# Kernel optimization log

Measured on AMD Instinct MI355X. Metric: run time of the kernel, lower is better.

The kernel has to match this reference:

```python
import jax, jax.numpy as jnp
import numpy as np

N_NODES = 50000
N_EDGES = 800000
IN_DIM, H1, H2 = 512, 128, 64


def setup_inputs() -> dict:
    key = jax.random.key(0)
    k1, k2, k3, k4 = jax.random.split(key, 4)
    x = jax.random.normal(k1, (N_NODES, IN_DIM), dtype=jnp.float32)
    edge_index = jax.random.randint(k2, (2, N_EDGES), 0, N_NODES, dtype=jnp.int64)
    # Glorot-ish scaled weights (PyG GCNConv uses glorot init)
    W1 = jax.random.normal(k3, (IN_DIM, H1), dtype=jnp.float32) * (1.0 / np.sqrt(IN_DIM))
    b1 = jnp.zeros((H1,), dtype=jnp.float32)
    W2 = jax.random.normal(k4, (H1, H2), dtype=jnp.float32) * (1.0 / np.sqrt(H1))
    b2 = jnp.zeros((H2,), dtype=jnp.float32)
    return {"x": x, "edge_index": edge_index, "W1": W1, "b1": b1, "W2": W2, "b2": b2}


def reference(x, edge_index, W1, b1, W2, b2):
    N = x.shape[0]
    # PyG GCNConv default: add self-loops + symmetric normalization
    loop = jnp.arange(N, dtype=edge_index.dtype)
    src = jnp.concatenate([edge_index[0], loop])  # message source j
    dst = jnp.concatenate([edge_index[1], loop])  # aggregation target i
    deg = jax.ops.segment_sum(jnp.ones(src.shape[0], dtype=x.dtype), dst, num_segments=N)
    dinv = jnp.where(deg > 0, jax.lax.rsqrt(deg), 0.0)
    norm = dinv[src] * dinv[dst]  # [E+N]

    def gcn_relu(h, W, b):
        h = h @ W                                   # [N, F_out]
        msg = h[src] * norm[:, None]                # gather + edge scaling
        agg = jax.ops.segment_sum(msg, dst, num_segments=N)  # scatter-add
        return jax.nn.relu(agg + b)

    h = gcn_relu(x, W1, b1)
    return gcn_relu(h, W2, b2)
```

## Files before the change

kernel.cpp:

```cpp
#include <hip/hip_runtime.h>


constexpr int IN_DIM = 512;
constexpr int HD1 = 128;
constexpr int HD2 = 64;

typedef __attribute__((ext_vector_type(8))) short bf16x8;
typedef __attribute__((ext_vector_type(8))) unsigned short u16x8;
typedef __attribute__((ext_vector_type(4))) float f32x4;
typedef unsigned int u32;

__device__ inline unsigned short f2bf(float f) {
    u32 u = __builtin_bit_cast(u32, f);
    return (unsigned short)((u + 0x7fffu + ((u >> 16) & 1u)) >> 16);
}
__device__ inline float bf_lo(u32 v) { return __builtin_bit_cast(float, v << 16); }
__device__ inline float bf_hi(u32 v) { return __builtin_bit_cast(float, v & 0xffff0000u); }

__device__ inline int elem_off(int row, int k) {
    return (row << 6) + (k ^ ((row & 7) << 3));
}
__device__ inline int elem_off128(int row, int k) {
    return (row << 7) + (k ^ ((row & 7) << 3));
}

__global__ __launch_bounds__(256) void k_zero(int* __restrict__ deg, int N) {
    int i = blockIdx.x * 256 + threadIdx.x;
    if (i < N) deg[i] = 0;
}

__global__ __launch_bounds__(256) void k_prep(const int* __restrict__ dst, int E,
                                              int* __restrict__ deg,
                                              int* __restrict__ rank,
                                              const float* __restrict__ W1,
                                              unsigned short* __restrict__ Wt,
                                              const float* __restrict__ W2,
                                              unsigned short* __restrict__ Wt2) {
    int id = blockIdx.x * 256 + threadIdx.x;
    if (id < E) rank[id] = atomicAdd(&deg[dst[id]], 1);
    if (id < IN_DIM * HD1) {
        int n = id >> 9, k = id & 511;
        Wt[id] = f2bf(W1[k * HD1 + n]);
    }
    if (id < HD1 * HD2) {
        int n = id >> 7, k = id & 127;
        Wt2[id] = f2bf(W2[k * HD2 + n]);
    }
}

__global__ __launch_bounds__(256) void k_dinv_bsum(const int* __restrict__ deg, int N,
                                                   float* __restrict__ dinv,
                                                   int* __restrict__ bsum) {
    __shared__ int s[256];
    int t = threadIdx.x;
    int i = blockIdx.x * 256 + t;
    int d = (i < N) ? deg[i] : 0;
    if (i < N) dinv[i] = rsqrtf((float)(d + 1));
    s[t] = d;
    __syncthreads();
    for (int st = 128; st > 0; st >>= 1) {
        if (t < st) s[t] += s[t + st];
        __syncthreads();
    }
    if (t == 0) bsum[blockIdx.x] = s[0];
}

__global__ __launch_bounds__(256) void k_scan_final(const int* __restrict__ deg, int N,
                                                    const int* __restrict__ bsum, int nb,
                                                    int* __restrict__ rowptr) {
    __shared__ int sb[256];
    __shared__ int s[256];
    int t = threadIdx.x;
    sb[t] = (t < nb) ? bsum[t] : 0;
    __syncthreads();
    for (int off = 1; off < 256; off <<= 1) {
        int v = (t >= off) ? sb[t - off] : 0;
        __syncthreads();
        sb[t] += v;
        __syncthreads();
    }
    int base = (blockIdx.x == 0) ? 0 : sb[blockIdx.x - 1];

    int i = blockIdx.x * 256 + t;
    int v = (i < N) ? deg[i] : 0;
    s[t] = v;
    __syncthreads();
    for (int off = 1; off < 256; off <<= 1) {
        int u = (t >= off) ? s[t - off] : 0;
        __syncthreads();
        s[t] += u;
        __syncthreads();
    }
    int incl = s[t] + base;
    if (i < N) rowptr[i] = incl - v;
    if (i == N - 1) rowptr[N] = incl;
}

__global__ __launch_bounds__(256) void k_mega(const float* __restrict__ X,
                                              const unsigned short* __restrict__ Wt,
                                              unsigned short* __restrict__ H, int N,
                                              int gemmBlocks,
                                              const int* __restrict__ src,
                                              const int* __restrict__ dst, int E,
                                              const int* __restrict__ rowptr,
                                              const int* __restrict__ rank,
                                              int* __restrict__ col) {
    __shared__ unsigned short As[32 * 64];
    __shared__ unsigned short Bs[128 * 64];

    if (blockIdx.x >= gemmBlocks) {
        const int T = (gridDim.x - gemmBlocks) * 256;
        for (int e = (blockIdx.x - gemmBlocks) * 256 + threadIdx.x; e < E; e += T) {
            int d = dst[e];
            col[rowptr[d] + rank[e]] = src[e];
        }
        return;
    }

    const int tid = threadIdx.x;
    const int lane = tid & 63;
    const int wid = tid >> 6;
    const int brow = blockIdx.x * 32;
    const int wr0 = (wid >> 1) * 16;
    const int wc0 = (wid & 1) * 64;
    const bool full = (brow + 32 <= N);

    f32x4 acc[4];
#pragma unroll
    for (int j = 0; j < 4; j++) acc[j] = (f32x4){0.f, 0.f, 0.f, 0.f};

    for (int kt = 0; kt < IN_DIM / 64; kt++) {
        const int k0 = kt * 64;
#pragma unroll
        for (int p = 0; p < 4; p++) {
            int chunk = (wid * 4 + p) * 64 + lane;
            int n = chunk >> 3;
            int kcs = chunk & 7;
            int kc = kcs ^ (n & 7);
            const unsigned short* srcp = &Wt[(size_t)n * IN_DIM + k0 + kc * 8];
            unsigned short* dstp = &Bs[(wid * 4 + p) * 512];
            __builtin_amdgcn_global_load_lds(
                (const __attribute__((address_space(1))) u32*)(const void*)srcp,
                (__attribute__((address_space(3))) u32*)(void*)dstp, 16, 0, 0);
        }
        {
            int r = tid >> 3;
            int kc = tid & 7;
            const float* xp = &X[(size_t)(brow + r) * IN_DIM + k0 + kc * 8];
            float4 v0, v1;
            if (full || (brow + r) < N) {
                v0 = *(const float4*)xp;
                v1 = *(const float4*)(xp + 4);
            } else {
                v0 = make_float4(0.f, 0.f, 0.f, 0.f); v1 = v0;
            }
            u16x8 w;
            w[0] = f2bf(v0.x); w[1] = f2bf(v0.y); w[2] = f2bf(v0.z); w[3] = f2bf(v0.w);
            w[4] = f2bf(v1.x); w[5] = f2bf(v1.y); w[6] = f2bf(v1.z); w[7] = f2bf(v1.w);
            *(u16x8*)&As[elem_off(r, kc * 8)] = w;
        }
        __syncthreads();

#pragma unroll
        for (int kk = 0; kk < 2; kk++) {
            const int kel = kk * 32 + (lane >> 4) * 8;
            bf16x8 a = *(const bf16x8*)&As[elem_off(wr0 + (lane & 15), kel)];
            bf16x8 b[4];
#pragma unroll
            for (int ni = 0; ni < 4; ni++)
                b[ni] = *(const bf16x8*)&Bs[elem_off(wc0 + ni * 16 + (lane & 15), kel)];
#pragma unroll
            for (int ni = 0; ni < 4; ni++)
                acc[ni] = __builtin_amdgcn_mfma_f32_16x16x32_bf16(a, b[ni], acc[ni], 0, 0, 0);
        }
        __syncthreads();
    }

#pragma unroll
    for (int reg = 0; reg < 4; reg++) {
        int grow = brow + wr0 + (lane >> 4) * 4 + reg;
        if (grow < N) {
#pragma unroll
            for (int ni = 0; ni < 4; ni++) {
                int gcol = wc0 + ni * 16 + (lane & 15);
                H[(size_t)grow * HD1 + gcol] = f2bf(acc[ni][reg]);
            }
        }
    }
}

__global__ __launch_bounds__(256) void k_gather1(const unsigned short* __restrict__ h,
                                                 const int* __restrict__ rowptr,
                                                 const int* __restrict__ col,
                                                 const float* __restrict__ dinv,
                                                 const float* __restrict__ bias,
                                                 unsigned short* __restrict__ out, int N) {
    const int i = (blockIdx.x * 256 + threadIdx.x) >> 6;
    const int lane = threadIdx.x & 63;
    if (i >= N) return;
    const int half = lane >> 5;
    const int c4 = (lane & 31) * 4;
    const float di = dinv[i];
    const unsigned short* hc = h + c4;

    float a0 = 0.f, a1 = 0.f, a2 = 0.f, a3 = 0.f;
    if (half == 0) {
        uint2 sv = *(const uint2*)&hc[(size_t)i * HD1];
        float s = di * di;
        a0 = bf_lo(sv.x) * s; a1 = bf_hi(sv.x) * s;
        a2 = bf_lo(sv.y) * s; a3 = bf_hi(sv.y) * s;
    }
    const int beg = rowptr[i], end = rowptr[i + 1];
    for (int p0 = beg; p0 < end; p0 += 64) {
        int idx = p0 + lane;
        bool okl = idx < end;
        int myj = okl ? col[idx] : i;
        float mydj = okl ? dinv[myj] : 0.f;
        const int cnt8 = (min(64, end - p0) + 7) & ~7;
        uint2 v[4]; float wv[4];
#pragma unroll
        for (int q = 0; q < 4; q++) {
            int e = 2 * q + half;
            int j = __shfl(myj, e);
            wv[q] = __shfl(mydj, e) * di;
            v[q] = *(const uint2*)&hc[(size_t)j * HD1];
        }
        for (int k = 8; k < cnt8; k += 8) {
            uint2 nv[4]; float nw[4];
#pragma unroll
            for (int q = 0; q < 4; q++) {
                int e = k + 2 * q + half;
                int j = __shfl(myj, e);
                nw[q] = __shfl(mydj, e) * di;
                nv[q] = *(const uint2*)&hc[(size_t)j * HD1];
            }
#pragma unroll
            for (int q = 0; q < 4; q++) {
                a0 = fmaf(bf_lo(v[q].x), wv[q], a0);
                a1 = fmaf(bf_hi(v[q].x), wv[q], a1);
                a2 = fmaf(bf_lo(v[q].y), wv[q], a2);
                a3 = fmaf(bf_hi(v[q].y), wv[q], a3);
            }
#pragma unroll
            for (int q = 0; q < 4; q++) { v[q] = nv[q]; wv[q] = nw[q]; }
        }
#pragma unroll
        for (int q = 0; q < 4; q++) {
            a0 = fmaf(bf_lo(v[q].x), wv[q], a0);
            a1 = fmaf(bf_hi(v[q].x), wv[q], a1);
            a2 = fmaf(bf_lo(v[q].y), wv[q], a2);
            a3 = fmaf(bf_hi(v[q].y), wv[q], a3);
        }
    }
    a0 += __shfl_xor(a0, 32);
    a1 += __shfl_xor(a1, 32);
    a2 += __shfl_xor(a2, 32);
    a3 += __shfl_xor(a3, 32);
    if (half == 0) {
        float4 bv = *(const float4*)&bias[c4];
        u32 w0 = (u32)f2bf(fmaxf(a0 + bv.x, 0.f)) | ((u32)f2bf(fmaxf(a1 + bv.y, 0.f)) << 16);
        u32 w1 = (u32)f2bf(fmaxf(a2 + bv.z, 0.f)) | ((u32)f2bf(fmaxf(a3 + bv.w, 0.f)) << 16);
        *(uint2*)&out[(size_t)i * HD1 + c4] = make_uint2(w0, w1);
    }
}

__global__ __launch_bounds__(256) void k_gemm2(const unsigned short* __restrict__ A,
                                               const unsigned short* __restrict__ Wt2,
                                               unsigned short* __restrict__ H, int N) {
    __shared__ unsigned short As[128 * 128];
    __shared__ unsigned short Bs[64 * 128];
    const int tid = threadIdx.x;
    const int lane = tid & 63;
    const int wid = tid >> 6;
    const int brow = blockIdx.x * 128;
    const int wr0 = wid * 32;

#pragma unroll
    for (int p = 0; p < 8; p++) {
        int chunk = (wid * 8 + p) * 64 + lane;
        int r = chunk >> 4;
        int kcs = chunk & 15;
        int kc = kcs ^ (r & 7);
        const unsigned short* src = &A[(size_t)(brow + r) * HD1 + kc * 8];
        unsigned short* dst = &As[(wid * 8 + p) * 512];
        __builtin_amdgcn_global_load_lds(
            (const __attribute__((address_space(1))) u32*)(const void*)src,
            (__attribute__((address_space(3))) u32*)(void*)dst, 16, 0, 0);
    }
#pragma unroll
    for (int p = 0; p < 4; p++) {
        int chunk = (wid * 4 + p) * 64 + lane;
        int c = chunk >> 4;
        int kcs = chunk & 15;
        int kc = kcs ^ (c & 7);
        const unsigned short* src = &Wt2[(size_t)c * HD1 + kc * 8];
        unsigned short* dst = &Bs[(wid * 4 + p) * 512];
        __builtin_amdgcn_global_load_lds(
            (const __attribute__((address_space(1))) u32*)(const void*)src,
            (__attribute__((address_space(3))) u32*)(void*)dst, 16, 0, 0);
    }
    __syncthreads();

    f32x4 acc[2][4];
#pragma unroll
    for (int i = 0; i < 2; i++)
#pragma unroll
        for (int j = 0; j < 4; j++) acc[i][j] = (f32x4){0.f, 0.f, 0.f, 0.f};

#pragma unroll
    for (int kk = 0; kk < 4; kk++) {
        const int kel = kk * 32 + (lane >> 4) * 8;
        bf16x8 a[2], b[4];
#pragma unroll
        for (int mi = 0; mi < 2; mi++)
            a[mi] = *(const bf16x8*)&As[elem_off128(wr0 + mi * 16 + (lane & 15), kel)];
#pragma unroll
        for (int ni = 0; ni < 4; ni++)
            b[ni] = *(const bf16x8*)&Bs[elem_off128(ni * 16 + (lane & 15), kel)];
#pragma unroll
        for (int mi = 0; mi < 2; mi++)
#pragma unroll
            for (int ni = 0; ni < 4; ni++)
                acc[mi][ni] = __builtin_amdgcn_mfma_f32_16x16x32_bf16(
                    a[mi], b[ni], acc[mi][ni], 0, 0, 0);
    }

#pragma unroll
    for (int mi = 0; mi < 2; mi++) {
#pragma unroll
        for (int reg = 0; reg < 4; reg++) {
            int grow = brow + wr0 + mi * 16 + (lane >> 4) * 4 + reg;
            if (grow < N) {
#pragma unroll
                for (int ni = 0; ni < 4; ni++) {
                    int gcol = ni * 16 + (lane & 15);
                    H[(size_t)grow * HD2 + gcol] = f2bf(acc[mi][ni][reg]);
                }
            }
        }
    }
}

__global__ __launch_bounds__(256) void k_gather2(const unsigned short* __restrict__ h,
                                                 const int* __restrict__ rowptr,
                                                 const int* __restrict__ col,
                                                 const float* __restrict__ dinv,
                                                 const float* __restrict__ bias,
                                                 float* __restrict__ out, int N) {
    const int i = (blockIdx.x * 256 + threadIdx.x) >> 6;
    const int lane = threadIdx.x & 63;
    if (i >= N) return;
    const int half = lane >> 5;
    const int c2 = (lane & 31) * 2;
    const float di = dinv[i];
    const unsigned short* hc = h + c2;

    float a0 = 0.f, a1 = 0.f;
    if (half == 0) {
        u32 sv = *(const u32*)&hc[(size_t)i * HD2];
        float s = di * di;
        a0 = bf_lo(sv) * s; a1 = bf_hi(sv) * s;
    }
    const int beg = rowptr[i], end = rowptr[i + 1];
    for (int p0 = beg; p0 < end; p0 += 64) {
        int idx = p0 + lane;
        bool okl = idx < end;
        int myj = okl ? col[idx] : i;
        float mydj = okl ? dinv[myj] : 0.f;
        const int cnt8 = (min(64, end - p0) + 7) & ~7;
        u32 v[4]; float wv[4];
#pragma unroll
        for (int q = 0; q < 4; q++) {
            int e = 2 * q + half;
            int j = __shfl(myj, e);
            wv[q] = __shfl(mydj, e) * di;
            v[q] = *(const u32*)&hc[(size_t)j * HD2];
        }
        for (int k = 8; k < cnt8; k += 8) {
            u32 nv[4]; float nw[4];
#pragma unroll
            for (int q = 0; q < 4; q++) {
                int e = k + 2 * q + half;
                int j = __shfl(myj, e);
                nw[q] = __shfl(mydj, e) * di;
                nv[q] = *(const u32*)&hc[(size_t)j * HD2];
            }
#pragma unroll
            for (int q = 0; q < 4; q++) {
                a0 = fmaf(bf_lo(v[q]), wv[q], a0);
                a1 = fmaf(bf_hi(v[q]), wv[q], a1);
            }
#pragma unroll
            for (int q = 0; q < 4; q++) { v[q] = nv[q]; wv[q] = nw[q]; }
        }
#pragma unroll
        for (int q = 0; q < 4; q++) {
            a0 = fmaf(bf_lo(v[q]), wv[q], a0);
            a1 = fmaf(bf_hi(v[q]), wv[q], a1);
        }
    }
    a0 += __shfl_xor(a0, 32);
    a1 += __shfl_xor(a1, 32);
    if (half == 0) {
        float2 bv = *(const float2*)&bias[c2];
        float2 r = make_float2(fmaxf(a0 + bv.x, 0.f), fmaxf(a1 + bv.y, 0.f));
        *(float2*)&out[(size_t)i * HD2 + c2] = r;
    }
}

extern "C" void kernel_launch(void* const* d_in, const int* in_sizes, int n_in,
                              void* d_out, int out_size, void* d_ws, size_t ws_size,
                              hipStream_t stream) {
    const float* x  = (const float*)d_in[0];
    const int*   ei = (const int*)d_in[1];
    const float* W1 = (const float*)d_in[2];
    const float* b1 = (const float*)d_in[3];
    const float* W2 = (const float*)d_in[4];
    const float* b2 = (const float*)d_in[5];
    float* out = (float*)d_out;

    const int N = in_sizes[0] / IN_DIM;
    const int E = in_sizes[1] / 2;
    const int* src = ei;
    const int* dst = ei + E;

    char* w = (char*)d_ws;
    size_t off = 0;
    auto alloc = [&](size_t bytes) -> void* {
        void* p = w + off;
        off = (off + bytes + 255) & ~(size_t)255;
        return p;
    };
    int*   deg    = (int*)alloc((size_t)N * 4);
    int*   rank   = (int*)alloc((size_t)E * 4);
    int*   rowptr = (int*)alloc((size_t)(N + 1) * 4);
    int*   bsum   = (int*)alloc(1024 * 4);
    int*   col    = (int*)alloc((size_t)E * 4);
    float* dinv   = (float*)alloc((size_t)N * 4);
    unsigned short* Wt  = (unsigned short*)alloc((size_t)IN_DIM * HD1 * 2);
    unsigned short* Wt2 = (unsigned short*)alloc((size_t)HD2 * HD1 * 2);
    unsigned short* h1  = (unsigned short*)alloc((size_t)N * HD1 * 2);
    unsigned short* agg1= (unsigned short*)alloc((size_t)(N + 128) * HD1 * 2);
    unsigned short* h2  = h1;

    const int nb = (N + 255) / 256;
    const int eb = (E + 255) / 256;
    const int gemmBlocks = (N + 31) / 32;
    const int fillBlocks = 512;

    k_zero<<<nb, 256, 0, stream>>>(deg, N);
    k_prep<<<eb, 256, 0, stream>>>(dst, E, deg, rank, W1, Wt, W2, Wt2);
    k_dinv_bsum<<<nb, 256, 0, stream>>>(deg, N, dinv, bsum);
    k_scan_final<<<nb, 256, 0, stream>>>(deg, N, bsum, nb, rowptr);

    k_mega<<<gemmBlocks + fillBlocks, 256, 0, stream>>>(
        x, Wt, h1, N, gemmBlocks, src, dst, E, rowptr, rank, col);

    k_gather1<<<(N * 64 + 255) / 256, 256, 0, stream>>>(h1, rowptr, col, dinv, b1, agg1, N);
    k_gemm2<<<(N + 127) / 128, 256, 0, stream>>>(agg1, Wt2, h2, N);
    k_gather2<<<(N * 64 + 255) / 256, 256, 0, stream>>>(h2, rowptr, col, dinv, b2, out, N);
}
```

Baseline: 145.2 us.

## Split hidden features into 32-column planes and gather each plane in separate passes

The GEMM epilogues now write H1 and H2 as column planes 32 features wide, each stored contiguously across all nodes. The gather kernels run one pass per plane (4 for layer 1, 2 for layer 2), and each wave handles one node's 64-byte slice with 4 edges in flight per load step. The aim is a smaller working set per pass (about 3.2 MB per plane) so the random neighbor gathers hit in L2/MALL more often. In exchange the col, rowptr and dinv arrays are re-read once per pass and many more waves are launched.

Result: slower. 204.2 us (+40.6%).

```diff
diff --git a/kernel.cpp b/kernel.cpp
--- a/kernel.cpp
+++ b/kernel.cpp
@@ -183,7 +183,9 @@
 #pragma unroll
             for (int ni = 0; ni < 4; ni++) {
                 int gcol = wc0 + ni * 16 + (lane & 15);
-                H[(size_t)grow * HD1 + gcol] = f2bf(acc[ni][reg]);
+                int plane = gcol >> 5;
+                H[(size_t)plane * N * 32 + (size_t)grow * 32 + (gcol & 31)] =
+                    f2bf(acc[ni][reg]);
             }
         }
     }
@@ -194,73 +196,57 @@
                                                  const int* __restrict__ col,
                                                  const float* __restrict__ dinv,
                                                  const float* __restrict__ bias,
-                                                 unsigned short* __restrict__ out, int N) {
-    const int i = (blockIdx.x * 256 + threadIdx.x) >> 6;
+                                                 unsigned short* __restrict__ out,
+                                                 int N, int PB) {
+    const int pass = blockIdx.x / PB;
+    const int lb = blockIdx.x - pass * PB;
+    const int i = (lb * 256 + threadIdx.x) >> 6;
     const int lane = threadIdx.x & 63;
     if (i >= N) return;
-    const int half = lane >> 5;
-    const int c4 = (lane & 31) * 4;
+    const int g = lane >> 4;
+    const int c2 = (lane & 15) * 2;
+    const unsigned short* hp = h + (size_t)pass * N * 32 + c2;
     const float di = dinv[i];
-    const unsigned short* hc = h + c4;
-
-    float a0 = 0.f, a1 = 0.f, a2 = 0.f, a3 = 0.f;
-    if (half == 0) {
-        uint2 sv = *(const uint2*)&hc[(size_t)i * HD1];
+
+    float a0 = 0.f, a1 = 0.f;
+    if (g == 0) {
+        u32 sv = *(const u32*)&hp[(size_t)i * 32];
         float s = di * di;
-        a0 = bf_lo(sv.x) * s; a1 = bf_hi(sv.x) * s;
-        a2 = bf_lo(sv.y) * s; a3 = bf_hi(sv.y) * s;
+        a0 = bf_lo(sv) * s; a1 = bf_hi(sv) * s;
     }
     const int beg = rowptr[i], end = rowptr[i + 1];
     for (int p0 = beg; p0 < end; p0 += 64) {
         int idx = p0 + lane;
-        bool okl = idx < end;
-        int myj = okl ? col[idx] : i;
-        float mydj = okl ? dinv[myj] : 0.f;
+        bool ok = idx < end;
+        int myj = ok ? col[idx] : i;
+        float mydj = ok ? dinv[myj] : 0.f;
         const int cnt8 = (min(64, end - p0) + 7) & ~7;
-        uint2 v[4]; float wv[4];
-#pragma unroll
-        for (int q = 0; q < 4; q++) {
-            int e = 2 * q + half;
-            int j = __shfl(myj, e);
-            wv[q] = __shfl(mydj, e) * di;
-            v[q] = *(const uint2*)&hc[(size_t)j * HD1];
+        u32 v0, v1; float w0, w1;
+        {
+            int j0 = __shfl(myj, g);     w0 = __shfl(mydj, g) * di;
+            v0 = *(const u32*)&hp[(size_t)j0 * 32];
+            int j1 = __shfl(myj, 4 + g); w1 = __shfl(mydj, 4 + g) * di;
+            v1 = *(const u32*)&hp[(size_t)j1 * 32];
         }
         for (int k = 8; k < cnt8; k += 8) {
-            uint2 nv[4]; float nw[4];
-#pragma unroll
-            for (int q = 0; q < 4; q++) {
-                int e = k + 2 * q + half;
-                int j = __shfl(myj, e);
-                nw[q] = __shfl(mydj, e) * di;
-                nv[q] = *(const uint2*)&hc[(size_t)j * HD1];
-            }
-#pragma unroll
-            for (int q = 0; q < 4; q++) {
-                a0 = fmaf(bf_lo(v[q].x), wv[q], a0);
-                a1 = fmaf(bf_hi(v[q].x), wv[q], a1);
-                a2 = fmaf(bf_lo(v[q].y), wv[q], a2);
-                a3 = fmaf(bf_hi(v[q].y), wv[q], a3);
-            }
-#pragma unroll
-            for (int q = 0; q < 4; q++) { v[q] = nv[q]; wv[q] = nw[q]; }
-        }
-#pragma unroll
-        for (int q = 0; q < 4; q++) {
-            a0 = fmaf(bf_lo(v[q].x), wv[q], a0);
-            a1 = fmaf(bf_hi(v[q].x), wv[q], a1);
-            a2 = fmaf(bf_lo(v[q].y), wv[q], a2);
-            a3 = fmaf(bf_hi(v[q].y), wv[q], a3);
-        }
-    }
-    a0 += __shfl_xor(a0, 32);
-    a1 += __shfl_xor(a1, 32);
-    a2 += __shfl_xor(a2, 32);
-    a3 += __shfl_xor(a3, 32);
-    if (half == 0) {
-        float4 bv = *(const float4*)&bias[c4];
-        u32 w0 = (u32)f2bf(fmaxf(a0 + bv.x, 0.f)) | ((u32)f2bf(fmaxf(a1 + bv.y, 0.f)) << 16);
-        u32 w1 = (u32)f2bf(fmaxf(a2 + bv.z, 0.f)) | ((u32)f2bf(fmaxf(a3 + bv.w, 0.f)) << 16);
-        *(uint2*)&out[(size_t)i * HD1 + c4] = make_uint2(w0, w1);
+            int j0 = __shfl(myj, k + g);     float nw0 = __shfl(mydj, k + g) * di;
+            u32 nv0 = *(const u32*)&hp[(size_t)j0 * 32];
+            int j1 = __shfl(myj, k + 4 + g); float nw1 = __shfl(mydj, k + 4 + g) * di;
+            u32 nv1 = *(const u32*)&hp[(size_t)j1 * 32];
+            a0 = fmaf(bf_lo(v0), w0, a0); a1 = fmaf(bf_hi(v0), w0, a1);
+            a0 = fmaf(bf_lo(v1), w1, a0); a1 = fmaf(bf_hi(v1), w1, a1);
+            v0 = nv0; w0 = nw0; v1 = nv1; w1 = nw1;
+        }
+        a0 = fmaf(bf_lo(v0), w0, a0); a1 = fmaf(bf_hi(v0), w0, a1);
+        a0 = fmaf(bf_lo(v1), w1, a0); a1 = fmaf(bf_hi(v1), w1, a1);
+    }
+    a0 += __shfl_xor(a0, 16); a1 += __shfl_xor(a1, 16);
+    a0 += __shfl_xor(a0, 32); a1 += __shfl_xor(a1, 32);
+    if (lane < 16) {
+        float2 bv = *(const float2*)&bias[pass * 32 + c2];
+        u32 w = (u32)f2bf(fmaxf(a0 + bv.x, 0.f)) |
+                ((u32)f2bf(fmaxf(a1 + bv.y, 0.f)) << 16);
+        *(u32*)&out[(size_t)i * HD1 + pass * 32 + c2] = w;
     }
 }
 
@@ -334,7 +320,9 @@
 #pragma unroll
                 for (int ni = 0; ni < 4; ni++) {
                     int gcol = ni * 16 + (lane & 15);
-                    H[(size_t)grow * HD2 + gcol] = f2bf(acc[mi][ni][reg]);
+                    int plane = gcol >> 5;
+                    H[(size_t)plane * N * 32 + (size_t)grow * 32 + (gcol & 31)] =
+                        f2bf(acc[mi][ni][reg]);
                 }
             }
         }
@@ -346,65 +334,56 @@
                                                  const int* __restrict__ col,
                                                  const float* __restrict__ dinv,
                                                  const float* __restrict__ bias,
-                                                 float* __restrict__ out, int N) {
-    const int i = (blockIdx.x * 256 + threadIdx.x) >> 6;
+                                                 float* __restrict__ out,
+                                                 int N, int PB) {
+    const int pass = blockIdx.x / PB;
+    const int lb = blockIdx.x - pass * PB;
+    const int i = (lb * 256 + threadIdx.x) >> 6;
     const int lane = threadIdx.x & 63;
     if (i >= N) return;
-    const int half = lane >> 5;
-    const int c2 = (lane & 31) * 2;
+    const int g = lane >> 4;
+    const int c2 = (lane & 15) * 2;
+    const unsigned short* hp = h + (size_t)pass * N * 32 + c2;
     const float di = dinv[i];
-    const unsigned short* hc = h + c2;
 
     float a0 = 0.f, a1 = 0.f;
-    if (half == 0) {
-        u32 sv = *(const u32*)&hc[(size_t)i * HD2];
+    if (g == 0) {
+        u32 sv = *(const u32*)&hp[(size_t)i * 32];
         float s = di * di;
         a0 = bf_lo(sv) * s; a1 = bf_hi(sv) * s;
     }
     const int beg = rowptr[i], end = rowptr[i + 1];
     for (int p0 = beg; p0 < end; p0 += 64) {
         int idx = p0 + lane;
-        bool okl = idx < end;
-        int myj = okl ? col[idx] : i;
-        float mydj = okl ? dinv[myj] : 0.f;
+        bool ok = idx < end;
+        int myj = ok ? col[idx] : i;
+        float mydj = ok ? dinv[myj] : 0.f;
         const int cnt8 = (min(64, end - p0) + 7) & ~7;
-        u32 v[4]; float wv[4];
-#pragma unroll
-        for (int q = 0; q < 4; q++) {
-            int e = 2 * q + half;
-            int j = __shfl(myj, e);
-            wv[q] = __shfl(mydj, e) * di;
-            v[q] = *(const u32*)&hc[(size_t)j * HD2];
+        u32 v0, v1; float w0, w1;
+        {
+            int j0 = __shfl(myj, g);     w0 = __shfl(mydj, g) * di;
+            v0 = *(const u32*)&hp[(size_t)j0 * 32];
+            int j1 = __shfl(myj, 4 + g); w1 = __shfl(mydj, 4 + g) * di;
+            v1 = *(const u32*)&hp[(size_t)j1 * 32];
         }
         for (int k = 8; k < cnt8; k += 8) {
-            u32 nv[4]; float nw[4];
-#pragma unroll
-            for (int q = 0; q < 4; q++) {
-                int e = k + 2 * q + half;
-                int j = __shfl(myj, e);
-                nw[q] = __shfl(mydj, e) * di;
-                nv[q] = *(const u32*)&hc[(size_t)j * HD2];
-            }
-#pragma unroll
-            for (int q = 0; q < 4; q++) {
-                a0 = fmaf(bf_lo(v[q]), wv[q], a0);
-                a1 = fmaf(bf_hi(v[q]), wv[q], a1);
-            }
-#pragma unroll
-            for (int q = 0; q < 4; q++) { v[q] = nv[q]; wv[q] = nw[q]; }
-        }
-#pragma unroll
-        for (int q = 0; q < 4; q++) {
-            a0 = fmaf(bf_lo(v[q]), wv[q], a0);
-            a1 = fmaf(bf_hi(v[q]), wv[q], a1);
-        }
-    }
-    a0 += __shfl_xor(a0, 32);
-    a1 += __shfl_xor(a1, 32);
-    if (half == 0) {
-        float2 bv = *(const float2*)&bias[c2];
+            int j0 = __shfl(myj, k + g);     float nw0 = __shfl(mydj, k + g) * di;
+            u32 nv0 = *(const u32*)&hp[(size_t)j0 * 32];
+            int j1 = __shfl(myj, k + 4 + g); float nw1 = __shfl(mydj, k + 4 + g) * di;
+            u32 nv1 = *(const u32*)&hp[(size_t)j1 * 32];
+            a0 = fmaf(bf_lo(v0), w0, a0); a1 = fmaf(bf_hi(v0), w0, a1);
+            a0 = fmaf(bf_lo(v1), w1, a0); a1 = fmaf(bf_hi(v1), w1, a1);
+            v0 = nv0; w0 = nw0; v1 = nv1; w1 = nw1;
+        }
+        a0 = fmaf(bf_lo(v0), w0, a0); a1 = fmaf(bf_hi(v0), w0, a1);
+        a0 = fmaf(bf_lo(v1), w1, a0); a1 = fmaf(bf_hi(v1), w1, a1);
+    }
+    a0 += __shfl_xor(a0, 16); a1 += __shfl_xor(a1, 16);
+    a0 += __shfl_xor(a0, 32); a1 += __shfl_xor(a1, 32);
+    if (lane < 16) {
+        float2 bv = *(const float2*)&bias[pass * 32 + c2];
         float2 r = make_float2(fmaxf(a0 + bv.x, 0.f), fmaxf(a1 + bv.y, 0.f));
-        *(float2*)&out[(size_t)i * HD2 + c2] = r;
+        *(float2*)&out[(size_t)i * HD2 + pass * 32 + c2] = r;
     }
 }
 
@@ -447,6 +426,7 @@
     const int eb = (E + 255) / 256;
     const int gemmBlocks = (N + 31) / 32;
     const int fillBlocks = 512;
+    const int PB = (N * 64 + 255) / 256;
 
     k_zero<<<nb, 256, 0, stream>>>(deg, N);
     k_prep<<<eb, 256, 0, stream>>>(dst, E, deg, rank, W1, Wt, W2, Wt2);
@@ -456,7 +436,7 @@
     k_mega<<<gemmBlocks + fillBlocks, 256, 0, stream>>>(
         x, Wt, h1, N, gemmBlocks, src, dst, E, rowptr, rank, col);
 
-    k_gather1<<<(N * 64 + 255) / 256, 256, 0, stream>>>(h1, rowptr, col, dinv, b1, agg1, N);
+    k_gather1<<<4 * PB, 256, 0, stream>>>(h1, rowptr, col, dinv, b1, agg1, N, PB);
     k_gemm2<<<(N + 127) / 128, 256, 0, stream>>>(agg1, Wt2, h2, N);
-    k_gather2<<<(N * 64 + 255) / 256, 256, 0, stream>>>(h2, rowptr, col, dinv, b2, out, N);
-}
+    k_gather2<<<2 * PB, 256, 0, stream>>>(h2, rowptr, col, dinv, b2, out, N, PB);
+}
```
